# Optimization experiments

Measured on AMD Instinct MI355X. Metric: run time of the kernel, lower is better.

Reference implementation:

```python
import jax, jax.numpy as jnp
import numpy as np

B, P, N, E, H, KD, M = 64, 100, 1000, 512, 8, 64, 10
SQRT_E = float(np.sqrt(E))
CLIP = 10.0


def _heads(x):
    # [b, n, H*KD] -> [b, H, n, KD]
    b, n, _ = x.shape
    return x.reshape(b, n, H, KD).transpose(0, 2, 1, 3)


def setup_inputs() -> dict:
    key = jax.random.key(0)
    ks = jax.random.split(key, 20)
    f = jnp.float32
    s = 0.02  # weight init scale
    return {
        "encoded_last_node": jax.random.normal(ks[0], (B, P, E), f),
        "encoded_last_agents": jax.random.normal(ks[1], (B, P, E), f),
        "cur_dist": jax.random.uniform(ks[2], (B, P, N), f, 1e-3, 1.0),
        "ninf_mask": jnp.zeros((B, P, N), f),
        "lengths": jax.random.uniform(ks[3], (B, P, M), f),
        "max_dis": jax.random.uniform(ks[4], (B, P, 1), f),
        "remain_max_dis": jax.random.uniform(ks[5], (B, P, 1), f),
        "q_first": 0.5 * jax.random.normal(ks[6], (B, H, P, KD), f),
        "k": 0.5 * jax.random.normal(ks[7], (B, H, N, KD), f),
        "v": 0.5 * jax.random.normal(ks[8], (B, H, N, KD), f),
        "single_head_key": 0.5 * jax.random.normal(ks[9], (B, E, N), f),
        "Wq_last_w": s * jax.random.normal(ks[10], (H * KD, 2 * E + 2), f),
        "dis_emb_w": s * jax.random.normal(ks[11], (H * KD, 4), f),
        "mh_w": s * jax.random.normal(ks[12], (E, H * KD), f),
        "mh_b": s * jax.random.normal(ks[13], (E,), f),
        "dist_alpha": jnp.ones((1,), f),
        "depot_num": jax.random.randint(ks[14], (B,), 1, M + 1),
        "route_cnt": jax.random.randint(ks[15], (B, P, 1), 0, M),
        "left_city": jax.random.randint(ks[16], (B, P), 0, N + 1),
        "city_num": N,
    }


def reference(encoded_last_node, encoded_last_agents, cur_dist, ninf_mask,
              lengths, max_dis, remain_max_dis, q_first, k, v, single_head_key,
              Wq_last_w, dis_emb_w, mh_w, mh_b, dist_alpha,
              depot_num, route_cnt, left_city, city_num):
    # route_num = depot_num - 1, broadcast to route_cnt shape [B,P,1]
    route_num = jnp.broadcast_to(depot_num[:, None, None], route_cnt.shape) - 1
    g_cur = jnp.take_along_axis(lengths, route_cnt, axis=-1)    # [B,P,1]
    g_route = jnp.take_along_axis(lengths, route_num, axis=-1)  # [B,P,1]
    q_info_in = jnp.concatenate([g_cur, g_route, max_dis, remain_max_dis], axis=-1)  # [B,P,4]
    q_info = _heads(q_info_in @ dis_emb_w.T)  # [B,H,P,KD]

    frac = 1.0 - (route_cnt + 1).astype(jnp.float32) / (route_num + 1).astype(jnp.float32)
    lc = left_city[:, :, None].astype(jnp.float32) / city_num
    q_last_in = jnp.concatenate([encoded_last_node, encoded_last_agents, frac, lc], axis=-1)  # [B,P,2E+2]
    q_last = _heads(q_last_in @ Wq_last_w.T)  # [B,H,P,KD]

    q = q_first + q_last + q_info  # [B,H,P,KD]

    # masked multi-head attention (rank3 ninf mask)
    score = jnp.einsum("bhpd,bhnd->bhpn", q, k) / jnp.sqrt(jnp.float32(KD))
    score = score + ninf_mask[:, None, :, :]
    w = jax.nn.softmax(score, axis=-1)
    out = jnp.einsum("bhpn,bhnd->bhpd", w, v)
    out_concat = out.transpose(0, 2, 1, 3).reshape(out.shape[0], out.shape[2], H * KD)  # [B,P,H*KD]
    mh = out_concat @ mh_w.T + mh_b  # [B,P,E]

    # single-head distance-biased scoring
    score2 = jnp.einsum("bpe,ben->bpn", mh, single_head_key)  # [B,P,N]
    max_dist = jnp.max(cur_dist, axis=-1, keepdims=True)
    cur_dist_out = -cur_dist / max_dist
    score_clipped = CLIP * jnp.tanh(score2 / SQRT_E + dist_alpha * cur_dist_out)
    probs = jax.nn.softmax(score_clipped + ninf_mask, axis=-1)
    return probs
```

## Files before the change

### kernel.cpp

```cpp
#include <hip/hip_runtime.h>
#include <hip/hip_bf16.h>

#define BB 64
#define PP 100
#define NN 1000
#define EE 512
#define HH 8
#define KDD 64
#define MM 10
#define ROWS (BB*PP)
#define K1K 1026
#define INVSQE 0.044194173824159216f
#define CLIPV 10.0f

union F4 { float4 v; float f[4]; };

using bf16x8 = __attribute__((ext_vector_type(8))) short;
using bf16x4 = __attribute__((ext_vector_type(4))) unsigned short;
using f32x4  = __attribute__((ext_vector_type(4))) float;

__device__ inline unsigned short f2bf(float x) {
  __hip_bfloat16 h = __float2bfloat16(x);
  unsigned short u;
  __builtin_memcpy(&u, &h, sizeof(u));
  return u;
}

__device__ inline float bf2f(unsigned short s) {
  return __uint_as_float(((unsigned)s) << 16);
}

__device__ inline float fast_tanh(float x) {
  float e = __expf(2.0f * x);
  return 1.0f - 2.0f / (e + 1.0f);
}

__global__ __launch_bounds__(256) void k_rowmax(const float* __restrict__ cd,
                                                float* __restrict__ rmax) {
  int row = blockIdx.x * 4 + (threadIdx.x >> 6);
  int lane = threadIdx.x & 63;
  const float* src = cd + (size_t)row * NN;
  float m = -1e30f;
  for (int i = lane; i < NN; i += 64) m = fmaxf(m, src[i]);
  #pragma unroll
  for (int off = 32; off; off >>= 1) m = fmaxf(m, __shfl_xor(m, off));
  if (lane == 0) rmax[row] = m;
}

__global__ __launch_bounds__(256) void k_qgemm(
    const float* __restrict__ eln, const float* __restrict__ ela,
    const float* __restrict__ lengths, const float* __restrict__ max_dis,
    const float* __restrict__ remain, const float* __restrict__ q_first,
    const float* __restrict__ Wq, const float* __restrict__ dis_emb,
    const int* __restrict__ depot, const int* __restrict__ route_cnt,
    const int* __restrict__ left_city, const int* __restrict__ city_num,
    float* __restrict__ qout) {
  __shared__ unsigned short Xs[64][40];
  __shared__ unsigned short Ws[64][40];
  __shared__ float info_s[64][4];
  __shared__ float fl_s[64][2];
  const int t = threadIdx.x;
  const int lane = t & 63;
  const int w = t >> 6;
  const int lr = lane & 15, lg = lane >> 4;
  const int rowBase = blockIdx.y * 64, colBase = blockIdx.x * 64;

  if (t < 64) {
    int row = rowBase + t;
    int b = row / PP;
    int rc = route_cnt[row];
    int rn = depot[b] - 1;
    info_s[t][0] = lengths[row * MM + rc];
    info_s[t][1] = lengths[row * MM + rn];
    info_s[t][2] = max_dis[row];
    info_s[t][3] = remain[row];
    fl_s[t][0] = 1.0f - (float)(rc + 1) / (float)(rn + 1);
    fl_s[t][1] = (float)left_city[row] / (float)city_num[0];
  }

  f32x4 acc[4];
  #pragma unroll
  for (int m = 0; m < 4; ++m) { acc[m][0] = 0.f; acc[m][1] = 0.f; acc[m][2] = 0.f; acc[m][3] = 0.f; }

  for (int kt = 0; kt < 32; ++kt) {
    const float* xsrc = (kt < 16) ? eln : ela;
    const int koff = (kt & 15) * 32;
    __syncthreads();
    #pragma unroll
    for (int i = 0; i < 2; ++i) {
      int s = i * 256 + t;
      int r = s >> 3, c4 = (s & 7) * 4;
      F4 xv, wv;
      xv.v = *(const float4*)&xsrc[(size_t)(rowBase + r) * 512 + koff + c4];
      wv.v = *(const float4*)&Wq[(size_t)(colBase + r) * K1K + kt * 32 + c4];
      unsigned short* xd = &Xs[r][c4];
      unsigned short* wd = &Ws[r][c4];
      xd[0] = f2bf(xv.f[0]); xd[1] = f2bf(xv.f[1]); xd[2] = f2bf(xv.f[2]); xd[3] = f2bf(xv.f[3]);
      wd[0] = f2bf(wv.f[0]); wd[1] = f2bf(wv.f[1]); wd[2] = f2bf(wv.f[2]); wd[3] = f2bf(wv.f[3]);
    }
    __syncthreads();
    bf16x8 bfr = *(bf16x8*)&Ws[w * 16 + lr][lg * 8];
    #pragma unroll
    for (int m = 0; m < 4; ++m) {
      bf16x8 af = *(bf16x8*)&Xs[m * 16 + lr][lg * 8];
      acc[m] = __builtin_amdgcn_mfma_f32_16x16x32_bf16(af, bfr, acc[m], 0, 0, 0);
    }
  }

  const int o = colBase + w * 16 + lr;
  F4 de; de.v = *(const float4*)&dis_emb[(size_t)o * 4];
  const float wq1024 = Wq[(size_t)o * K1K + 1024];
  const float wq1025 = Wq[(size_t)o * K1K + 1025];
  const int h = o >> 6, kd = o & 63;
  #pragma unroll
  for (int m = 0; m < 4; ++m) {
    #pragma unroll
    for (int j = 0; j < 4; ++j) {
      int r = m * 16 + lg * 4 + j;
      int row = rowBase + r;
      int b = row / PP, p = row % PP;
      F4 inf; inf.v = *(const float4*)&info_s[r][0];
      float v = acc[m][j]
              + inf.f[0] * de.f[0] + inf.f[1] * de.f[1]
              + inf.f[2] * de.f[2] + inf.f[3] * de.f[3]
              + fl_s[r][0] * wq1024 + fl_s[r][1] * wq1025
              + q_first[(((size_t)b * HH + h) * PP + p) * KDD + kd];
      qout[(size_t)row * 512 + o] = v;
    }
  }
}

__global__ __launch_bounds__(256) void k_attn(
    const float* __restrict__ qin, const float* __restrict__ kk,
    const float* __restrict__ vv, const float* __restrict__ mask,
    float* __restrict__ attn_out) {
  __shared__ unsigned short Kl[64][72];
  __shared__ unsigned short Vt[64][72];
  __shared__ unsigned short PMb[64][72];

  const int t = threadIdx.x;
  const int lane = t & 63;
  const int w = t >> 6;
  const int lr = lane & 15, lg = lane >> 4;
  const int gid = blockIdx.x;
  const int b = gid & 63;
  const int X = gid >> 6;
  const int h = X & 7, half = X >> 3;
  const int bh = b * HH + h;
  const int p0 = half * 64;
  const int nrows = (half == 0) ? 64 : (PP - 64);
  const bool active = (w * 16 < nrows);

  #pragma unroll
  for (int i = 0; i < 4; ++i) {
    int idx = i * 256 + t;
    int r = idx >> 4, c4 = (idx & 15) * 4;
    int p = p0 + r;
    F4 qv; qv.v = make_float4(0.f, 0.f, 0.f, 0.f);
    if (p < PP) qv.v = *(const float4*)&qin[((size_t)(b * PP + p)) * 512 + h * 64 + c4];
    unsigned short* d = &PMb[r][c4];
    d[0] = f2bf(qv.f[0] * 0.125f); d[1] = f2bf(qv.f[1] * 0.125f);
    d[2] = f2bf(qv.f[2] * 0.125f); d[3] = f2bf(qv.f[3] * 0.125f);
  }
  __syncthreads();

  bf16x8 qf[2];
  qf[0] = *(bf16x8*)&PMb[w * 16 + lr][lg * 8];
  qf[1] = *(bf16x8*)&PMb[w * 16 + lr][32 + lg * 8];
  __syncthreads();

  float Lacc[4] = {0.f, 0.f, 0.f, 0.f};
  f32x4 Oa[4];
  #pragma unroll
  for (int dt = 0; dt < 4; ++dt) { Oa[dt][0] = 0.f; Oa[dt][1] = 0.f; Oa[dt][2] = 0.f; Oa[dt][3] = 0.f; }

  for (int ch = 0; ch < 16; ++ch) {
    const int n0 = ch * 64;

    #pragma unroll
    for (int i = 0; i < 4; ++i) {
      int idx = i * 256 + t;
      int r = idx >> 4, c4 = (idx & 15) * 4;
      int n = n0 + r;
      F4 kv; kv.v = make_float4(0.f, 0.f, 0.f, 0.f);
      if (n < NN) kv.v = *(const float4*)&kk[(((size_t)bh * NN) + n) * 64 + c4];
      unsigned short* d = &Kl[r][c4];
      d[0] = f2bf(kv.f[0]); d[1] = f2bf(kv.f[1]); d[2] = f2bf(kv.f[2]); d[3] = f2bf(kv.f[3]);
    }
    {
      int b2 = t & 15, a = t >> 4;
      F4 rowv[4];
      #pragma unroll
      for (int r = 0; r < 4; ++r) {
        int n = n0 + 4 * b2 + r;
        rowv[r].v = (n < NN) ? *(const float4*)&vv[(((size_t)bh * NN) + n) * 64 + 4 * a]
                             : make_float4(0.f, 0.f, 0.f, 0.f);
      }
      #pragma unroll
      for (int c = 0; c < 4; ++c) {
        unsigned short* dst = &Vt[4 * a + c][4 * b2];
        dst[0] = f2bf(rowv[0].f[c]); dst[1] = f2bf(rowv[1].f[c]);
        dst[2] = f2bf(rowv[2].f[c]); dst[3] = f2bf(rowv[3].f[c]);
      }
    }
    #pragma unroll
    for (int i = 0; i < 4; ++i) {
      int idx = i * 256 + t;
      int r = idx >> 4, c4 = (idx & 15) * 4;
      if (r < nrows) {
        int p = p0 + r, n = n0 + c4;
        F4 mv;
        if (n + 3 < NN) {
          mv.v = *(const float4*)&mask[((size_t)(b * PP + p)) * NN + n];
        } else {
          #pragma unroll
          for (int j = 0; j < 4; ++j)
            mv.f[j] = (n + j < NN) ? mask[((size_t)(b * PP + p)) * NN + n + j] : -1e30f;
        }
        unsigned short* d = &PMb[r][c4];
        d[0] = f2bf(mv.f[0]); d[1] = f2bf(mv.f[1]); d[2] = f2bf(mv.f[2]); d[3] = f2bf(mv.f[3]);
      }
    }
    __syncthreads();

    if (active) {
      f32x4 sa[4];
      #pragma unroll
      for (int nb = 0; nb < 4; ++nb) { sa[nb][0] = 0.f; sa[nb][1] = 0.f; sa[nb][2] = 0.f; sa[nb][3] = 0.f; }
      #pragma unroll
      for (int kb = 0; kb < 2; ++kb)
        #pragma unroll
        for (int nb = 0; nb < 4; ++nb) {
          bf16x8 kf = *(bf16x8*)&Kl[nb * 16 + lr][kb * 32 + lg * 8];
          sa[nb] = __builtin_amdgcn_mfma_f32_16x16x32_bf16(qf[kb], kf, sa[nb], 0, 0, 0);
        }
      #pragma unroll
      for (int j = 0; j < 4; ++j) {
        int pr = w * 16 + lg * 4 + j;
        #pragma unroll
        for (int nb = 0; nb < 4; ++nb) {
          float mv = bf2f(PMb[pr][nb * 16 + lr]);
          float e = __expf(sa[nb][j] + mv);
          Lacc[j] += e;
          PMb[pr][nb * 16 + lr] = f2bf(e);
        }
      }
      #pragma unroll
      for (int kb = 0; kb < 2; ++kb) {
        bf16x8 pf = *(bf16x8*)&PMb[w * 16 + lr][kb * 32 + lg * 8];
        #pragma unroll
        for (int dt = 0; dt < 4; ++dt) {
          bf16x8 vf = *(bf16x8*)&Vt[dt * 16 + lr][kb * 32 + lg * 8];
          Oa[dt] = __builtin_amdgcn_mfma_f32_16x16x32_bf16(pf, vf, Oa[dt], 0, 0, 0);
        }
      }
    }
    __syncthreads();
  }

  if (active) {
    #pragma unroll
    for (int j = 0; j < 4; ++j) {
      float L = Lacc[j];
      #pragma unroll
      for (int off = 1; off < 16; off <<= 1) L += __shfl_xor(L, off);
      int p = p0 + w * 16 + lg * 4 + j;
      if (p < PP) {
        float inv = (L > 0.f) ? 1.0f / L : 0.f;
        #pragma unroll
        for (int dt = 0; dt < 4; ++dt)
          attn_out[((size_t)(b * PP + p)) * 512 + h * 64 + dt * 16 + lr] = Oa[dt][j] * inv;
      }
    }
  }
}

__global__ __launch_bounds__(256) void k_mhgemm(
    const float* __restrict__ A, const float* __restrict__ W,
    const float* __restrict__ bias, float* __restrict__ out) {
  __shared__ unsigned short Xs[64][40];
  __shared__ unsigned short Ws[64][40];
  const int t = threadIdx.x;
  const int lane = t & 63;
  const int w = t >> 6;
  const int lr = lane & 15, lg = lane >> 4;
  const int rowBase = blockIdx.y * 64, colBase = blockIdx.x * 64;

  f32x4 acc[4];
  #pragma unroll
  for (int m = 0; m < 4; ++m) { acc[m][0] = 0.f; acc[m][1] = 0.f; acc[m][2] = 0.f; acc[m][3] = 0.f; }

  for (int kt = 0; kt < 16; ++kt) {
    const int koff = kt * 32;
    __syncthreads();
    #pragma unroll
    for (int i = 0; i < 2; ++i) {
      int s = i * 256 + t;
      int r = s >> 3, c4 = (s & 7) * 4;
      F4 xv, wv;
      xv.v = *(const float4*)&A[(size_t)(rowBase + r) * 512 + koff + c4];
      wv.v = *(const float4*)&W[(size_t)(colBase + r) * 512 + koff + c4];
      unsigned short* xd = &Xs[r][c4];
      unsigned short* wd = &Ws[r][c4];
      xd[0] = f2bf(xv.f[0]); xd[1] = f2bf(xv.f[1]); xd[2] = f2bf(xv.f[2]); xd[3] = f2bf(xv.f[3]);
      wd[0] = f2bf(wv.f[0]); wd[1] = f2bf(wv.f[1]); wd[2] = f2bf(wv.f[2]); wd[3] = f2bf(wv.f[3]);
    }
    __syncthreads();
    bf16x8 bfr = *(bf16x8*)&Ws[w * 16 + lr][lg * 8];
    #pragma unroll
    for (int m = 0; m < 4; ++m) {
      bf16x8 af = *(bf16x8*)&Xs[m * 16 + lr][lg * 8];
      acc[m] = __builtin_amdgcn_mfma_f32_16x16x32_bf16(af, bfr, acc[m], 0, 0, 0);
    }
  }

  const int o = colBase + w * 16 + lr;
  const float bv = bias[o];
  #pragma unroll
  for (int m = 0; m < 4; ++m) {
    #pragma unroll
    for (int j = 0; j < 4; ++j) {
      int row = rowBase + m * 16 + lg * 4 + j;
      out[(size_t)row * 512 + o] = acc[m][j] + bv;
    }
  }
}

__global__ __launch_bounds__(256) void k_final_score(
    const float* __restrict__ mh, const float* __restrict__ shk,
    const float* __restrict__ cur_dist, const float* __restrict__ rmax,
    const float* __restrict__ mask, const float* __restrict__ dist_alpha,
    float* __restrict__ sc_out) {
  __shared__ unsigned short As[112][40];
  __shared__ unsigned short Bt[64][40];
  const int t = threadIdx.x;
  const int lane = t & 63;
  const int w = t >> 6;
  const int lr = lane & 15, lg = lane >> 4;
  const int n0 = blockIdx.x * 64, b = blockIdx.y;

  f32x4 acc[7];
  #pragma unroll
  for (int m = 0; m < 7; ++m) { acc[m][0] = 0.f; acc[m][1] = 0.f; acc[m][2] = 0.f; acc[m][3] = 0.f; }

  for (int kt = 0; kt < 16; ++kt) {
    const int k0 = kt * 32;
    __syncthreads();
    #pragma unroll
    for (int i = 0; i < 4; ++i) {
      int s = i * 256 + t;
      if (s < 896) {
        int r = s >> 3, c4 = (s & 7) * 4;
        F4 xv; xv.v = make_float4(0.f, 0.f, 0.f, 0.f);
        if (r < PP) xv.v = *(const float4*)&mh[(size_t)(b * PP + r) * 512 + k0 + c4];
        unsigned short* xd = &As[r][c4];
        xd[0] = f2bf(xv.f[0]); xd[1] = f2bf(xv.f[1]); xd[2] = f2bf(xv.f[2]); xd[3] = f2bf(xv.f[3]);
      }
    }
    if (t < 128) {
      int a = t & 15, kb = t >> 4;
      F4 rowv[4];
      #pragma unroll
      for (int r = 0; r < 4; ++r) {
        int k = k0 + 4 * kb + r;
        int n = n0 + 4 * a;
        rowv[r].v = (n < NN) ? *(const float4*)&shk[((size_t)b * EE + k) * NN + n]
                             : make_float4(0.f, 0.f, 0.f, 0.f);
      }
      #pragma unroll
      for (int c = 0; c < 4; ++c) {
        unsigned short* dst = &Bt[4 * a + c][4 * kb];
        dst[0] = f2bf(rowv[0].f[c]); dst[1] = f2bf(rowv[1].f[c]);
        dst[2] = f2bf(rowv[2].f[c]); dst[3] = f2bf(rowv[3].f[c]);
      }
    }
    __syncthreads();
    bf16x8 bfr = *(bf16x8*)&Bt[w * 16 + lr][lg * 8];
    #pragma unroll
    for (int m = 0; m < 7; ++m) {
      bf16x8 af = *(bf16x8*)&As[m * 16 + lr][lg * 8];
      acc[m] = __builtin_amdgcn_mfma_f32_16x16x32_bf16(af, bfr, acc[m], 0, 0, 0);
    }
  }

  const float alpha = dist_alpha[0];
  const int n = n0 + w * 16 + lr;
  if (n < NN) {
    #pragma unroll
    for (int m = 0; m < 7; ++m) {
      #pragma unroll
      for (int j = 0; j < 4; ++j) {
        int p = m * 16 + lg * 4 + j;
        if (p >= PP) continue;
        size_t rb = (size_t)(b * PP + p) * NN;
        float rmx = rmax[b * PP + p];
        float cd = cur_dist[rb + n];
        float mk = mask[rb + n];
        sc_out[rb + n] = CLIPV * fast_tanh(acc[m][j] * INVSQE - alpha * cd / rmx) + mk;
      }
    }
  }
}

__global__ __launch_bounds__(256) void k_softmax(const float* __restrict__ sc,
                                                 float* __restrict__ out) {
  __shared__ float redm[4];
  __shared__ float redsum[4];
  const int row = blockIdx.x;
  const int t = threadIdx.x;
  const float* src = sc + (size_t)row * NN;
  float v0[4];
  float m = -1e30f;
  #pragma unroll
  for (int i = 0; i < 4; ++i) {
    int n = i * 256 + t;
    v0[i] = (n < NN) ? src[n] : -1e30f;
    m = fmaxf(m, v0[i]);
  }
  #pragma unroll
  for (int off = 32; off; off >>= 1) m = fmaxf(m, __shfl_xor(m, off));
  int wid = t >> 6, lane = t & 63;
  if (lane == 0) redm[wid] = m;
  __syncthreads();
  m = fmaxf(fmaxf(redm[0], redm[1]), fmaxf(redm[2], redm[3]));
  float e[4];
  float s = 0.f;
  #pragma unroll
  for (int i = 0; i < 4; ++i) {
    int n = i * 256 + t;
    e[i] = (n < NN) ? __expf(v0[i] - m) : 0.f;
    s += e[i];
  }
  #pragma unroll
  for (int off = 32; off; off >>= 1) s += __shfl_xor(s, off);
  if (lane == 0) redsum[wid] = s;
  __syncthreads();
  s = redsum[0] + redsum[1] + redsum[2] + redsum[3];
  float inv = 1.0f / s;
  #pragma unroll
  for (int i = 0; i < 4; ++i) {
    int n = i * 256 + t;
    if (n < NN) out[(size_t)row * NN + n] = e[i] * inv;
  }
}

extern "C" void kernel_launch(void* const* d_in, const int* in_sizes, int n_in,
                              void* d_out, int out_size, void* d_ws, size_t ws_size,
                              hipStream_t stream) {
  const float* eln       = (const float*)d_in[0];
  const float* ela       = (const float*)d_in[1];
  const float* cur_dist  = (const float*)d_in[2];
  const float* ninf      = (const float*)d_in[3];
  const float* lengths   = (const float*)d_in[4];
  const float* max_dis   = (const float*)d_in[5];
  const float* remain    = (const float*)d_in[6];
  const float* q_first   = (const float*)d_in[7];
  const float* kten      = (const float*)d_in[8];
  const float* vten      = (const float*)d_in[9];
  const float* shk       = (const float*)d_in[10];
  const float* Wq        = (const float*)d_in[11];
  const float* dis_emb   = (const float*)d_in[12];
  const float* mh_w      = (const float*)d_in[13];
  const float* mh_b      = (const float*)d_in[14];
  const float* dalpha    = (const float*)d_in[15];
  const int*   depot     = (const int*)d_in[16];
  const int*   route_cnt = (const int*)d_in[17];
  const int*   left_city = (const int*)d_in[18];
  const int*   city_num  = (const int*)d_in[19];
  float* out = (float*)d_out;

  float* ws      = (float*)d_ws;
  float* q_ws    = ws;
  float* attn_ws = q_ws + (size_t)ROWS * 512;
  float* mh_ws   = attn_ws + (size_t)ROWS * 512;
  float* sc_ws   = mh_ws + (size_t)ROWS * 512;
  float* rmax_ws = sc_ws + (size_t)ROWS * NN;

  k_rowmax<<<ROWS / 4, 256, 0, stream>>>(cur_dist, rmax_ws);
  k_qgemm<<<dim3(8, 100), 256, 0, stream>>>(eln, ela, lengths, max_dis, remain,
                                            q_first, Wq, dis_emb, depot, route_cnt,
                                            left_city, city_num, q_ws);
  k_attn<<<1024, 256, 0, stream>>>(q_ws, kten, vten, ninf, attn_ws);
  k_mhgemm<<<dim3(8, 100), 256, 0, stream>>>(attn_ws, mh_w, mh_b, mh_ws);
  k_final_score<<<dim3(16, 64), 256, 0, stream>>>(mh_ws, shk, cur_dist, rmax_ws,
                                                  ninf, dalpha, sc_ws);
  k_softmax<<<ROWS, 256, 0, stream>>>(sc_ws, out);
}
```

Measured before the change: 308.2 us.

## Process all 100 query rows per (batch, head) block in attention kernel

The attention kernel now uses 512-thread blocks, one per (batch, head), covering all 100 query rows with 7 active waves instead of splitting the rows across two blocks. Each K/V chunk is therefore loaded and converted to bf16 once per head rather than twice, which halves K/V global traffic. LDS stores are packed into vector writes, and the mask/probability tiles use a permuted column layout so each lane handles 4 contiguous bf16 values. The trade-offs are half as many blocks and one idle wave per block, which may lower occupancy and latency hiding.

Measured after the change: 320.5 us. 4.0% more time.

```diff
diff --git a/kernel.cpp b/kernel.cpp
--- a/kernel.cpp
+++ b/kernel.cpp
@@ -130,13 +130,13 @@
   }
 }
 
-__global__ __launch_bounds__(256) void k_attn(
+__global__ __launch_bounds__(512) void k_attn(
     const float* __restrict__ qin, const float* __restrict__ kk,
     const float* __restrict__ vv, const float* __restrict__ mask,
     float* __restrict__ attn_out) {
   __shared__ unsigned short Kl[64][72];
   __shared__ unsigned short Vt[64][72];
-  __shared__ unsigned short PMb[64][72];
+  __shared__ unsigned short PMb[112][72];
 
   const int t = threadIdx.x;
   const int lane = t & 63;
@@ -144,29 +144,32 @@
   const int lr = lane & 15, lg = lane >> 4;
   const int gid = blockIdx.x;
   const int b = gid & 63;
-  const int X = gid >> 6;
-  const int h = X & 7, half = X >> 3;
+  const int h = gid >> 6;
   const int bh = b * HH + h;
-  const int p0 = half * 64;
-  const int nrows = (half == 0) ? 64 : (PP - 64);
-  const bool active = (w * 16 < nrows);
+  const bool active = (w < 7);
+  const int vb = t & 31, va = t >> 5;
+  const int vlr = vb & 15, vpair = vb >> 4;
 
   #pragma unroll
   for (int i = 0; i < 4; ++i) {
-    int idx = i * 256 + t;
-    int r = idx >> 4, c4 = (idx & 15) * 4;
-    int p = p0 + r;
-    F4 qv; qv.v = make_float4(0.f, 0.f, 0.f, 0.f);
-    if (p < PP) qv.v = *(const float4*)&qin[((size_t)(b * PP + p)) * 512 + h * 64 + c4];
-    unsigned short* d = &PMb[r][c4];
-    d[0] = f2bf(qv.f[0] * 0.125f); d[1] = f2bf(qv.f[1] * 0.125f);
-    d[2] = f2bf(qv.f[2] * 0.125f); d[3] = f2bf(qv.f[3] * 0.125f);
+    int idx = i * 512 + t;
+    if (idx < 1792) {
+      int r = idx >> 4, c4 = (idx & 15) * 4;
+      F4 qv; qv.v = make_float4(0.f, 0.f, 0.f, 0.f);
+      if (r < PP) qv.v = *(const float4*)&qin[((size_t)(b * PP + r)) * 512 + h * 64 + c4];
+      bf16x4 pk;
+      pk[0] = f2bf(qv.f[0] * 0.125f); pk[1] = f2bf(qv.f[1] * 0.125f);
+      pk[2] = f2bf(qv.f[2] * 0.125f); pk[3] = f2bf(qv.f[3] * 0.125f);
+      *(bf16x4*)&PMb[r][c4] = pk;
+    }
   }
   __syncthreads();
 
   bf16x8 qf[2];
-  qf[0] = *(bf16x8*)&PMb[w * 16 + lr][lg * 8];
-  qf[1] = *(bf16x8*)&PMb[w * 16 + lr][32 + lg * 8];
+  if (active) {
+    qf[0] = *(bf16x8*)&PMb[w * 16 + lr][lg * 8];
+    qf[1] = *(bf16x8*)&PMb[w * 16 + lr][32 + lg * 8];
+  }
   __syncthreads();
 
   float Lacc[4] = {0.f, 0.f, 0.f, 0.f};
@@ -178,47 +181,47 @@
     const int n0 = ch * 64;
 
     #pragma unroll
-    for (int i = 0; i < 4; ++i) {
-      int idx = i * 256 + t;
+    for (int i = 0; i < 2; ++i) {
+      int idx = i * 512 + t;
       int r = idx >> 4, c4 = (idx & 15) * 4;
       int n = n0 + r;
       F4 kv; kv.v = make_float4(0.f, 0.f, 0.f, 0.f);
       if (n < NN) kv.v = *(const float4*)&kk[(((size_t)bh * NN) + n) * 64 + c4];
-      unsigned short* d = &Kl[r][c4];
-      d[0] = f2bf(kv.f[0]); d[1] = f2bf(kv.f[1]); d[2] = f2bf(kv.f[2]); d[3] = f2bf(kv.f[3]);
+      bf16x4 pk;
+      pk[0] = f2bf(kv.f[0]); pk[1] = f2bf(kv.f[1]);
+      pk[2] = f2bf(kv.f[2]); pk[3] = f2bf(kv.f[3]);
+      *(bf16x4*)&Kl[r][c4] = pk;
     }
     {
-      int b2 = t & 15, a = t >> 4;
-      F4 rowv[4];
-      #pragma unroll
-      for (int r = 0; r < 4; ++r) {
-        int n = n0 + 4 * b2 + r;
-        rowv[r].v = (n < NN) ? *(const float4*)&vv[(((size_t)bh * NN) + n) * 64 + 4 * a]
-                             : make_float4(0.f, 0.f, 0.f, 0.f);
-      }
+      int k1 = n0 + vlr + vpair * 32;
+      int k2 = k1 + 16;
+      F4 v1, v2;
+      v1.v = (k1 < NN) ? *(const float4*)&vv[(((size_t)bh * NN) + k1) * 64 + 4 * va]
+                       : make_float4(0.f, 0.f, 0.f, 0.f);
+      v2.v = (k2 < NN) ? *(const float4*)&vv[(((size_t)bh * NN) + k2) * 64 + 4 * va]
+                       : make_float4(0.f, 0.f, 0.f, 0.f);
       #pragma unroll
       for (int c = 0; c < 4; ++c) {
-        unsigned short* dst = &Vt[4 * a + c][4 * b2];
-        dst[0] = f2bf(rowv[0].f[c]); dst[1] = f2bf(rowv[1].f[c]);
-        dst[2] = f2bf(rowv[2].f[c]); dst[3] = f2bf(rowv[3].f[c]);
+        unsigned pv = (unsigned)f2bf(v1.f[c]) | ((unsigned)f2bf(v2.f[c]) << 16);
+        *(unsigned*)&Vt[va * 4 + c][vlr * 4 + vpair * 2] = pv;
       }
     }
     #pragma unroll
     for (int i = 0; i < 4; ++i) {
-      int idx = i * 256 + t;
-      int r = idx >> 4, c4 = (idx & 15) * 4;
-      if (r < nrows) {
-        int p = p0 + r, n = n0 + c4;
-        F4 mv;
-        if (n + 3 < NN) {
-          mv.v = *(const float4*)&mask[((size_t)(b * PP + p)) * NN + n];
-        } else {
-          #pragma unroll
-          for (int j = 0; j < 4; ++j)
-            mv.f[j] = (n + j < NN) ? mask[((size_t)(b * PP + p)) * NN + n + j] : -1e30f;
+      int idx = i * 512 + t;
+      if (idx < 1792) {
+        int r = idx >> 4, g = idx & 15;
+        bf16x4 pk;
+        #pragma unroll
+        for (int q = 0; q < 4; ++q) {
+          int n = n0 + g + q * 16;
+          float mval;
+          if (n >= NN) mval = -1e30f;
+          else if (r < PP) mval = mask[((size_t)(b * PP + r)) * NN + n];
+          else mval = 0.f;
+          pk[q] = f2bf(mval);
         }
-        unsigned short* d = &PMb[r][c4];
-        d[0] = f2bf(mv.f[0]); d[1] = f2bf(mv.f[1]); d[2] = f2bf(mv.f[2]); d[3] = f2bf(mv.f[3]);
+        *(bf16x4*)&PMb[r][g * 4] = pk;
       }
     }
     __syncthreads();
@@ -237,13 +240,15 @@
       #pragma unroll
       for (int j = 0; j < 4; ++j) {
         int pr = w * 16 + lg * 4 + j;
-        #pragma unroll
-        for (int nb = 0; nb < 4; ++nb) {
-          float mv = bf2f(PMb[pr][nb * 16 + lr]);
-          float e = __expf(sa[nb][j] + mv);
-          Lacc[j] += e;
-          PMb[pr][nb * 16 + lr] = f2bf(e);
-        }
+        bf16x4 mv4 = *(bf16x4*)&PMb[pr][lr * 4];
+        float e0 = __expf(sa[0][j] + bf2f(mv4[0]));
+        float e1 = __expf(sa[1][j] + bf2f(mv4[1]));
+        float e2 = __expf(sa[2][j] + bf2f(mv4[2]));
+        float e3 = __expf(sa[3][j] + bf2f(mv4[3]));
+        Lacc[j] += (e0 + e1) + (e2 + e3);
+        bf16x4 ev;
+        ev[0] = f2bf(e0); ev[1] = f2bf(e1); ev[2] = f2bf(e2); ev[3] = f2bf(e3);
+        *(bf16x4*)&PMb[pr][lr * 4] = ev;
       }
       #pragma unroll
       for (int kb = 0; kb < 2; ++kb) {
@@ -264,7 +269,7 @@
       float L = Lacc[j];
       #pragma unroll
       for (int off = 1; off < 16; off <<= 1) L += __shfl_xor(L, off);
-      int p = p0 + w * 16 + lg * 4 + j;
+      int p = w * 16 + lg * 4 + j;
       if (p < PP) {
         float inv = (L > 0.f) ? 1.0f / L : 0.f;
         #pragma unroll
@@ -480,7 +485,7 @@
   k_qgemm<<<dim3(8, 100), 256, 0, stream>>>(eln, ela, lengths, max_dis, remain,
                                             q_first, Wq, dis_emb, depot, route_cnt,
                                             left_city, city_num, q_ws);
-  k_attn<<<1024, 256, 0, stream>>>(q_ws, kten, vten, ninf, attn_ws);
+  k_attn<<<512, 512, 0, stream>>>(q_ws, kten, vten, ninf, attn_ws);
   k_mhgemm<<<dim3(8, 100), 256, 0, stream>>>(attn_ws, mh_w, mh_b, mh_ws);
   k_final_score<<<dim3(16, 64), 256, 0, stream>>>(mh_ws, shk, cur_dist, rmax_ws,
                                                   ninf, dalpha, sc_ws);
```

## Split attention over key dimension into two partitions with merge kernel

Applied to the files above, without the earlier changes.

Splits the attention kernel along the N (key) axis into two partial blocks, doubling the grid from 1024 to 2048 workgroups. Each partial block writes unnormalized bf16 outputs and row sums, and a new merge kernel adds the two partitions and normalizes. The aim is more parallelism and better occupancy on the GPU. The cost is an extra launch, an extra round trip through memory, and bf16 rounding of the partial outputs. Summing the partials without rescaling relies on the softmax exponentials not being max-subtracted per partition, which the unseen code presumably ensures.

Result: slower. 321.2 us (+4.2%).

```diff
diff --git a/kernel.cpp b/kernel.cpp
--- a/kernel.cpp
+++ b/kernel.cpp
@@ -130,10 +130,10 @@
   }
 }
 
-__global__ __launch_bounds__(256) void k_attn(
+__global__ __launch_bounds__(256) void k_attn_part(
     const float* __restrict__ qin, const float* __restrict__ kk,
     const float* __restrict__ vv, const float* __restrict__ mask,
-    float* __restrict__ attn_out) {
+    unsigned short* __restrict__ pO, float* __restrict__ pl) {
   __shared__ unsigned short Kl[64][72];
   __shared__ unsigned short Vt[64][72];
   __shared__ unsigned short PMb[64][72];
@@ -145,7 +145,9 @@
   const int gid = blockIdx.x;
   const int b = gid & 63;
   const int X = gid >> 6;
-  const int h = X & 7, half = X >> 3;
+  const int h = X & 7;
+  const int half = (X >> 3) & 1;
+  const int part = X >> 4;
   const int bh = b * HH + h;
   const int p0 = half * 64;
   const int nrows = (half == 0) ? 64 : (PP - 64);
@@ -174,8 +176,8 @@
   #pragma unroll
   for (int dt = 0; dt < 4; ++dt) { Oa[dt][0] = 0.f; Oa[dt][1] = 0.f; Oa[dt][2] = 0.f; Oa[dt][3] = 0.f; }
 
-  for (int ch = 0; ch < 16; ++ch) {
-    const int n0 = ch * 64;
+  for (int cc = 0; cc < 8; ++cc) {
+    const int n0 = (part * 8 + cc) * 64;
 
     #pragma unroll
     for (int i = 0; i < 4; ++i) {
@@ -264,15 +266,37 @@
       float L = Lacc[j];
       #pragma unroll
       for (int off = 1; off < 16; off <<= 1) L += __shfl_xor(L, off);
-      int p = p0 + w * 16 + lg * 4 + j;
+      int plocal = w * 16 + lg * 4 + j;
+      int p = p0 + plocal;
       if (p < PP) {
-        float inv = (L > 0.f) ? 1.0f / L : 0.f;
         #pragma unroll
         for (int dt = 0; dt < 4; ++dt)
-          attn_out[((size_t)(b * PP + p)) * 512 + h * 64 + dt * 16 + lr] = Oa[dt][j] * inv;
-      }
-    }
-  }
+          pO[(size_t)gid * 4096 + plocal * 64 + dt * 16 + lr] = f2bf(Oa[dt][j]);
+        if (lr == 0) pl[gid * 64 + plocal] = L;
+      }
+    }
+  }
+}
+
+__global__ __launch_bounds__(256) void k_attn_merge(
+    const unsigned short* __restrict__ pO, const float* __restrict__ pl,
+    float* __restrict__ attn_out) {
+  const int rid = blockIdx.x * 4 + (threadIdx.x >> 6);
+  const int d = threadIdx.x & 63;
+  const int b = rid / (HH * PP);
+  const int rem = rid % (HH * PP);
+  const int h = rem / PP, p = rem % PP;
+  const int half = (p >= 64) ? 1 : 0;
+  const int plocal = p - half * 64;
+  float O = 0.f, L = 0.f;
+  #pragma unroll
+  for (int part = 0; part < 2; ++part) {
+    int gid = ((part * 16 + half * 8 + h) << 6) | b;
+    O += bf2f(pO[(size_t)gid * 4096 + plocal * 64 + d]);
+    L += pl[gid * 64 + plocal];
+  }
+  float inv = (L > 0.f) ? 1.0f / L : 0.f;
+  attn_out[((size_t)(b * PP + p)) * 512 + h * 64 + d] = O * inv;
 }
 
 __global__ __launch_bounds__(256) void k_mhgemm(
@@ -476,11 +500,15 @@
   float* sc_ws   = mh_ws + (size_t)ROWS * 512;
   float* rmax_ws = sc_ws + (size_t)ROWS * NN;
 
+  unsigned short* pO_ws = (unsigned short*)mh_ws;
+  float* pl_ws = mh_ws + (size_t)4194304;
+
   k_rowmax<<<ROWS / 4, 256, 0, stream>>>(cur_dist, rmax_ws);
   k_qgemm<<<dim3(8, 100), 256, 0, stream>>>(eln, ela, lengths, max_dis, remain,
                                             q_first, Wq, dis_emb, depot, route_cnt,
                                             left_city, city_num, q_ws);
-  k_attn<<<1024, 256, 0, stream>>>(q_ws, kten, vten, ninf, attn_ws);
+  k_attn_part<<<2048, 256, 0, stream>>>(q_ws, kten, vten, ninf, pO_ws, pl_ws);
+  k_attn_merge<<<(ROWS * HH) / 4, 256, 0, stream>>>(pO_ws, pl_ws, attn_ws);
   k_mhgemm<<<dim3(8, 100), 256, 0, stream>>>(attn_ws, mh_w, mh_b, mh_ws);
   k_final_score<<<dim3(16, 64), 256, 0, stream>>>(mh_ws, shk, cur_dist, rmax_ws,
                                                   ninf, dalpha, sc_ws);
```
